# Optimization experiments

Measured on AMD Instinct MI355X. Metric: run time of the kernel, lower is better.

## Reference

```python
import jax, jax.numpy as jnp
import numpy as np

N = 50000
E = 800000
IN_C = 128
HID = 32
OUT_C = 16
NEG_SLOPE = 0.2


def setup_inputs() -> dict:
    key = jax.random.key(0)
    ks = jax.random.split(key, 16)
    x = jax.random.normal(ks[0], (N, IN_C), dtype=jnp.float32)
    edge_index = jax.random.randint(ks[1], (2, E), 0, N, dtype=jnp.int64)

    def glorot(k, shape):
        fan = shape[0] + shape[-1]
        return jax.random.uniform(k, shape, jnp.float32, -1.0, 1.0) * jnp.sqrt(6.0 / fan)

    # layer1: in=128 -> heads=4, ch=32, concat -> out 128
    W1 = glorot(ks[2], (IN_C, 4 * HID))
    a_src1 = glorot(ks[3], (4, HID))
    a_dst1 = glorot(ks[4], (4, HID))
    b1 = jnp.zeros((4 * HID,), jnp.float32)
    # layer2: in=128 -> heads=2, ch=32, concat -> out 64
    W2 = glorot(ks[5], (4 * HID, 2 * HID))
    a_src2 = glorot(ks[6], (2, HID))
    a_dst2 = glorot(ks[7], (2, HID))
    b2 = jnp.zeros((2 * HID,), jnp.float32)
    # layer3: in=64 -> heads=1, ch=16, mean -> out 16
    W3 = glorot(ks[8], (2 * HID, OUT_C))
    a_src3 = glorot(ks[9], (1, OUT_C))
    a_dst3 = glorot(ks[10], (1, OUT_C))
    b3 = jnp.zeros((OUT_C,), jnp.float32)
    return {"x": x, "edge_index": edge_index,
            "W1": W1, "a_src1": a_src1, "a_dst1": a_dst1, "b1": b1,
            "W2": W2, "a_src2": a_src2, "a_dst2": a_dst2, "b2": b2,
            "W3": W3, "a_src3": a_src3, "a_dst3": a_dst3, "b3": b3}


def gat_conv(x, src, dst, W, a_src, a_dst, bias, heads, ch, concat):
    n = x.shape[0]
    h = (x @ W).reshape(n, heads, ch)                      # [N,H,C]
    alpha_s = jnp.einsum('nhc,hc->nh', h, a_src)           # [N,H]
    alpha_d = jnp.einsum('nhc,hc->nh', h, a_dst)           # [N,H]
    logits = jax.nn.leaky_relu(alpha_s[src] + alpha_d[dst], NEG_SLOPE)  # [E,H]
    # segment softmax over edges sharing the same destination node
    m = jax.ops.segment_max(logits, dst, num_segments=n)
    m = jnp.where(jnp.isfinite(m), m, 0.0)
    e = jnp.exp(logits - m[dst])
    denom = jax.ops.segment_sum(e, dst, num_segments=n)
    alpha = e / (denom[dst] + 1e-16)                       # [E,H]
    msg = h[src] * alpha[:, :, None]                       # [E,H,C]
    out = jax.ops.segment_sum(msg, dst, num_segments=n)    # [N,H,C]
    out = out.reshape(n, heads * ch) if concat else out.mean(axis=1)
    return out + bias


def reference(x, edge_index, W1, a_src1, a_dst1, b1, W2, a_src2, a_dst2, b2, W3, a_src3, a_dst3, b3):
    n = x.shape[0]
    loops = jnp.arange(n, dtype=edge_index.dtype)
    src = jnp.concatenate([edge_index[0], loops])  # add self loops (PyG default)
    dst = jnp.concatenate([edge_index[1], loops])
    h = jax.nn.relu(gat_conv(x, src, dst, W1, a_src1, a_dst1, b1, 4, HID, True))
    h = jax.nn.relu(gat_conv(h, src, dst, W2, a_src2, a_dst2, b2, 2, HID, True))
    out = gat_conv(h, src, dst, W3, a_src3, a_dst3, b3, 1, OUT_C, False)
    return out
```

## Files before the change

### kernel.cpp

```cpp
#include <hip/hip_runtime.h>
#include <hip/hip_bf16.h>
#include <stdint.h>

#define NODES 50000
#define NEDGE 800000
#define TEDGE (NEDGE + NODES)
#define SBLK 25

typedef unsigned short u16;
typedef unsigned int u32;
typedef unsigned long long u64;
typedef short s16x8 __attribute__((ext_vector_type(8)));
typedef float f32x4 __attribute__((ext_vector_type(4)));

__device__ __forceinline__ float bf2f(u16 v) {
  return __uint_as_float(((u32)v) << 16);
}
__device__ __forceinline__ u16 f2bf(float f) {
  u32 u = __float_as_uint(f);
  u32 r = (u + 0x7FFFu + ((u >> 16) & 1u)) >> 16;
  return (u16)r;
}
__device__ __forceinline__ float lo16f(u32 w) { return __uint_as_float(w << 16); }
__device__ __forceinline__ float hi16f(u32 w) { return __uint_as_float(w & 0xFFFF0000u); }
__device__ __forceinline__ float lrelu(float x) {
  return (x > 0.f) ? x : 0.2f * x;
}
__device__ __forceinline__ int clampn(int v) {
  return ((u32)v < NODES) ? v : 0;
}
__device__ __forceinline__ float load1(const void* p, size_t i, bool fb) {
  return fb ? bf2f(((const u16*)p)[i]) : ((const float*)p)[i];
}
__device__ __forceinline__ u32 encf(float f) {
  u32 u = __float_as_uint(f);
  return (u & 0x80000000u) ? ~u : (u | 0x80000000u);
}
__device__ __forceinline__ float decf(u32 k) {
  u32 u = (k & 0x80000000u) ? (k & 0x7FFFFFFFu) : ~k;
  return __uint_as_float(u);
}

__global__ __launch_bounds__(256) void k_probe(
    const int* __restrict__ ei, const u16* __restrict__ xs16,
    int* __restrict__ flags, int* __restrict__ deg,
    const void* __restrict__ W1, const void* __restrict__ W2,
    const void* __restrict__ W3, const void* __restrict__ as1,
    const void* __restrict__ ad1, const void* __restrict__ as2,
    const void* __restrict__ ad2, const void* __restrict__ as3,
    const void* __restrict__ ad3, u16* __restrict__ wt1,
    u16* __restrict__ wt2, u16* __restrict__ wt3, u16* __restrict__ wa1,
    u16* __restrict__ wa2, u16* __restrict__ wa3) {
  __shared__ int sfb;
  int t = threadIdx.x;
  int g = blockIdx.x * 256 + t;
  if (g < NODES) deg[g] = 0;
  if (blockIdx.x == 0 && t >= 2 && t < 32) flags[t] = 0;
  if (t < 64) {
    int big = 0;
#pragma unroll
    for (int k = 0; k < 4; ++k) {
      u32 ex = (xs16[2 * (t * 4 + k)] >> 7) & 0xFF;
      big += (ex >= 0x90);
    }
#pragma unroll
    for (int off = 32; off >= 1; off >>= 1) big += __shfl_xor(big, off);
    if (t == 0) sfb = (big >= 8) ? 0 : 1;
    if (blockIdx.x == 0) {
      int odd = 0, even = 0;
#pragma unroll
      for (int k = 0; k < 4; ++k) {
        int idx = t + 64 * k;
        odd |= (ei[2 * idx + 1] != 0);
        even |= (ei[2 * idx] != 0);
      }
      u64 bo = __ballot(odd);
      u64 be = __ballot(even);
      if (t == 0) flags[0] = (bo == 0ull && be != 0ull) ? 1 : 0;
    }
  }
  __syncthreads();
  bool fb = sfb != 0;
  if (blockIdx.x == 0 && t == 0) flags[1] = fb ? 1 : 0;

  auto fidx = [](int n, int k, int KS) {
    int nt = n >> 4, lrow = n & 15, ks = k >> 5, quad = (k >> 3) & 3, j = k & 7;
    return ((size_t)((nt * KS + ks) * 64 + quad * 16 + lrow)) * 8 + j;
  };

  if (g < 16384) {
    int n = g >> 7, k = g & 127;
    wt1[fidx(n, k, 4)] = f2bf(load1(W1, (size_t)k * 128 + n, fb));
  } else if (g < 24576) {
    int r = g - 16384;
    int n = r >> 7, k = r & 127;
    wt2[fidx(n, k, 4)] = f2bf(load1(W2, (size_t)k * 64 + n, fb));
  } else if (g < 25600) {
    int r = g - 24576;
    int n = r >> 6, k = r & 63;
    wt3[fidx(n, k, 2)] = f2bf(load1(W3, (size_t)k * 16 + n, fb));
  } else if (g < 27648) {
    int e = g - 25600;
    int n = e >> 7, k = e & 127;
    float v = 0.f;
    if (n < 8) {
      int head = (n < 4) ? n : n - 4;
      const void* av = (n < 4) ? as1 : ad1;
      for (int c = 0; c < 32; ++c)
        v += load1(W1, (size_t)k * 128 + head * 32 + c, fb) *
             load1(av, head * 32 + c, fb);
    }
    wa1[fidx(n, k, 4)] = (n < 8) ? f2bf(v) : (u16)0;
  } else if (g < 29696) {
    int e = g - 27648;
    int n = e >> 7, k = e & 127;
    float v = 0.f;
    if (n < 4) {
      int head = (n < 2) ? n : n - 2;
      const void* av = (n < 2) ? as2 : ad2;
      for (int c = 0; c < 32; ++c)
        v += load1(W2, (size_t)k * 64 + head * 32 + c, fb) *
             load1(av, head * 32 + c, fb);
    }
    wa2[fidx(n, k, 4)] = (n < 4) ? f2bf(v) : (u16)0;
  } else if (g < 30720) {
    int e = g - 29696;
    int n = e >> 6, k = e & 63;
    float v = 0.f;
    if (n < 2) {
      const void* av = (n < 1) ? as3 : ad3;
      for (int c = 0; c < 16; ++c)
        v += load1(W3, (size_t)k * 16 + c, fb) * load1(av, c, fb);
    }
    wa3[fidx(n, k, 2)] = (n < 2) ? f2bf(v) : (u16)0;
  }
}

__global__ __launch_bounds__(256) void k_hist(const int* __restrict__ ei,
                                              const int* __restrict__ flags,
                                              int* deg, u16* __restrict__ rankarr,
                                              u16* __restrict__ src16,
                                              u16* __restrict__ dst16) {
  int e = blockIdx.x * 256 + threadIdx.x;
  if (e >= TEDGE) return;
  int d, s;
  if (e < NEDGE) {
    if (flags[0]) { s = ei[2 * e]; d = ei[2 * (NEDGE + e)]; }
    else { s = ei[e]; d = ei[NEDGE + e]; }
  } else {
    s = e - NEDGE; d = s;
  }
  s = clampn(s); d = clampn(d);
  src16[e] = (u16)s;
  dst16[e] = (u16)d;
  int r = atomicAdd(&deg[d], 1);
  rankarr[e] = (u16)min(r, 65535);
}

__global__ __launch_bounds__(1024) void k_scan(const int* __restrict__ deg,
                                               int* __restrict__ rowptr,
                                               int* __restrict__ parts,
                                               int* __restrict__ counter) {
  __shared__ int swave[16];
  __shared__ int sbase, stot;
  int b = blockIdx.x, t = threadIdx.x;
  int lane = t & 63, w = t >> 6;
  int i0 = b * 2048 + t * 2;
  int v0 = (i0 < NODES) ? deg[i0] : 0;
  int v1 = (i0 + 1 < NODES) ? deg[i0 + 1] : 0;
  int local = v0 + v1;
  int x = local;
#pragma unroll
  for (int off = 1; off < 64; off <<= 1) {
    int y = __shfl_up(x, off);
    if (lane >= off) x += y;
  }
  if (lane == 63) swave[w] = x;
  __syncthreads();
  if (w == 0) {
    int wv = (lane < 16) ? swave[lane] : 0;
#pragma unroll
    for (int off = 1; off < 16; off <<= 1) {
      int y = __shfl_up(wv, off);
      if (lane >= off) wv += y;
    }
    if (lane == 15) {
      __hip_atomic_store(&parts[b], wv, __ATOMIC_RELAXED,
                         __HIP_MEMORY_SCOPE_AGENT);
      __hip_atomic_fetch_add(counter, 1, __ATOMIC_RELEASE,
                             __HIP_MEMORY_SCOPE_AGENT);
    }
    if (lane < 16) swave[lane] = wv;
  }
  __syncthreads();
  if (t == 0) {
    while (__hip_atomic_load(counter, __ATOMIC_ACQUIRE,
                             __HIP_MEMORY_SCOPE_AGENT) < SBLK)
      __builtin_amdgcn_s_sleep(2);
  }
  __syncthreads();
  if (w == 0) {
    int pv = (lane < SBLK) ? __hip_atomic_load(&parts[lane], __ATOMIC_RELAXED,
                                               __HIP_MEMORY_SCOPE_AGENT)
                           : 0;
    int pb = (lane < b) ? pv : 0;
#pragma unroll
    for (int off = 32; off >= 1; off >>= 1) {
      pb += __shfl_xor(pb, off);
      pv += __shfl_xor(pv, off);
    }
    if (lane == 0) { sbase = pb; stot = pv; }
  }
  __syncthreads();
  int run = sbase + ((w == 0) ? 0 : swave[w - 1]) + (x - local);
  if (i0 < NODES) rowptr[i0] = run;
  if (i0 + 1 < NODES) rowptr[i0 + 1] = run + v0;
  if (b == 0 && t == 0) rowptr[NODES] = stot;
}

__global__ __launch_bounds__(256) void k_scatter(const u16* __restrict__ src16,
                                                 const u16* __restrict__ dst16,
                                                 const int* __restrict__ rowptr,
                                                 const u16* __restrict__ rankarr,
                                                 u16* __restrict__ srcs) {
  int e = blockIdx.x * 256 + threadIdx.x;
  if (e >= TEDGE) return;
  int d = dst16[e];
  int pos = rowptr[d] + (int)rankarr[e];
  srcs[pos] = src16[e];
}

template <int K, int N, int H, bool XEXT>
__global__ __launch_bounds__(256) void k_gmfma(const void* __restrict__ xin,
                                               const u16* __restrict__ wtf,
                                               const u16* __restrict__ waf,
                                               u16* __restrict__ hout,
                                               float* __restrict__ asg,
                                               float* __restrict__ adg,
                                               u32* __restrict__ gm,
                                               const int* __restrict__ flags,
                                               int M) {
  constexpr int NT = N / 16;
  constexpr int KS = K / 32;
  __shared__ u32 lmax[2 * H];
  int t = threadIdx.x;
  int lane = t & 63, w = t >> 6;
  int lrow = lane & 15, quad = lane >> 4;
  bool fb = flags[1] != 0;
  if (t < 2 * H) lmax[t] = 0;
  __syncthreads();

  int row0 = blockIdx.x * 128 + w * 32;
  f32x4 acc[2][NT];
  f32x4 eacc[2];
#pragma unroll
  for (int mt = 0; mt < 2; ++mt) {
    eacc[mt] = (f32x4){0.f, 0.f, 0.f, 0.f};
#pragma unroll
    for (int nt = 0; nt < NT; ++nt) acc[mt][nt] = (f32x4){0.f, 0.f, 0.f, 0.f};
  }
  int r0c = row0 + lrow;
  int r1c = row0 + 16 + lrow;
  if (r0c >= M) r0c = M - 1;
  if (r1c >= M) r1c = M - 1;

#pragma unroll 1
  for (int ks = 0; ks < KS; ++ks) {
    s16x8 bw[NT];
#pragma unroll
    for (int nt = 0; nt < NT; ++nt)
      bw[nt] = *(const s16x8*)(wtf + ((size_t)((nt * KS + ks) * 64 + lane)) * 8);
    s16x8 be = *(const s16x8*)(waf + ((size_t)(ks * 64 + lane)) * 8);
#pragma unroll
    for (int mt = 0; mt < 2; ++mt) {
      int grow = mt ? r1c : r0c;
      s16x8 a;
      if (XEXT && !fb) {
        const float* gp = (const float*)xin + (size_t)grow * K + ks * 32 + quad * 8;
        float4 f0 = *(const float4*)gp;
        float4 f1 = *(const float4*)(gp + 4);
        a[0] = (short)f2bf(f0.x); a[1] = (short)f2bf(f0.y);
        a[2] = (short)f2bf(f0.z); a[3] = (short)f2bf(f0.w);
        a[4] = (short)f2bf(f1.x); a[5] = (short)f2bf(f1.y);
        a[6] = (short)f2bf(f1.z); a[7] = (short)f2bf(f1.w);
      } else {
        a = *(const s16x8*)((const u16*)xin + (size_t)grow * K + ks * 32 + quad * 8);
      }
#pragma unroll
      for (int nt = 0; nt < NT; ++nt)
        acc[mt][nt] =
            __builtin_amdgcn_mfma_f32_16x16x32_bf16(a, bw[nt], acc[mt][nt], 0, 0, 0);
      eacc[mt] = __builtin_amdgcn_mfma_f32_16x16x32_bf16(a, be, eacc[mt], 0, 0, 0);
    }
  }

  float pm = -3.4e38f;
#pragma unroll
  for (int mt = 0; mt < 2; ++mt) {
    int baserow = row0 + mt * 16 + quad * 4;
#pragma unroll
    for (int r = 0; r < 4; ++r) {
      int grow = baserow + r;
      if (grow < M) {
#pragma unroll
        for (int nt = 0; nt < NT; ++nt)
          hout[(size_t)grow * N + nt * 16 + lrow] = f2bf(acc[mt][nt][r]);
        if (lrow < H) asg[grow * H + lrow] = eacc[mt][r];
        else if (lrow < 2 * H) adg[grow * H + (lrow - H)] = eacc[mt][r];
      }
      pm = fmaxf(pm, eacc[mt][r]);
    }
  }
  if (lrow < 2 * H) atomicMax(&lmax[lrow], encf(pm));
  __syncthreads();
  if (t < 2 * H) atomicMax(&gm[t], lmax[t]);
}

template <int H, int C, bool RELU, bool FINAL>
__global__ __launch_bounds__(256) void k_agg(const u16* __restrict__ hbuf,
                                             const float* __restrict__ asg,
                                             const float* __restrict__ adg,
                                             const int* __restrict__ rowptr,
                                             const u16* __restrict__ srcs,
                                             const void* __restrict__ bias,
                                             const int* __restrict__ flags,
                                             const u32* __restrict__ gm,
                                             void* __restrict__ outp, int n) {
  constexpr int HC = H * C;
  constexpr int L = HC / 8;
  constexpr int EPN = 32 / L;
  constexpr int UN = (4 * EPN <= 32) ? 4 : 2;
  __shared__ u16 lds_s[4][64];
  __shared__ float lds_e[4][64][H];
  int lane = threadIdx.x & 63;
  int w = threadIdx.x >> 6;
  int nh = lane >> 5;
  int hl = lane & 31;
  int node = blockIdx.x * 8 + w * 2 + nh;
  if (node >= n) node = n - 1;
  bool fb = flags[1] != 0;
  int start = rowptr[node], end = rowptr[node + 1];
  if (end < start || end - start > TEDGE) { start = 0; end = 0; }

  float adh[H], M[H];
#pragma unroll
  for (int h = 0; h < H; ++h) adh[h] = adg[node * H + h];
#pragma unroll
  for (int h = 0; h < H; ++h) M[h] = lrelu(decf(gm[h]) + decf(gm[H + h]));

  int sub = hl / L;
  int cl = hl & (L - 1);
  int ch0 = cl * 8;
  int myhead = ch0 / C;
  int base = nh * 32;

  float den[H];
#pragma unroll
  for (int h = 0; h < H; ++h) den[h] = 0.f;
  float acc[UN][8];
#pragma unroll
  for (int u = 0; u < UN; ++u)
#pragma unroll
    for (int i = 0; i < 8; ++i) acc[u][i] = 0.f;

  for (int chunk = start; chunk < end; chunk += 32) {
    int e = chunk + hl;
    int s = 0;
    float ee[H];
#pragma unroll
    for (int h = 0; h < H; ++h) ee[h] = 0.f;
    if (e < end) {
      s = srcs[e];
      float av[H];
      if (H == 4) { float4 t4 = *(const float4*)(asg + s * 4);
        av[0] = t4.x; av[1] = t4.y; av[H > 2 ? 2 : 0] = t4.z; av[H > 3 ? 3 : 0] = t4.w; }
      else if (H == 2) { float2 t2 = *(const float2*)(asg + s * 2); av[0] = t2.x; av[1] = t2.y; }
      else av[0] = asg[s];
#pragma unroll
      for (int h = 0; h < H; ++h) {
        float x = __expf(lrelu(av[h] + adh[h]) - M[h]);
        ee[h] = x;
        den[h] += x;
      }
    }
    __builtin_amdgcn_wave_barrier();
    lds_s[w][lane] = (u16)s;
#pragma unroll
    for (int h = 0; h < H; ++h) lds_e[w][lane][h] = ee[h];
    __builtin_amdgcn_wave_barrier();

    int cn = min(32, end - chunk);
    for (int j = 0; j < cn; j += UN * EPN) {
      int sx[UN];
      float ax[UN];
#pragma unroll
      for (int u = 0; u < UN; ++u) {
        int ei_ = base + j + u * EPN + sub;
        sx[u] = lds_s[w][ei_];
        ax[u] = lds_e[w][ei_][myhead];
      }
#pragma unroll
      for (int u = 0; u < UN; ++u) {
        uint4 v = *(const uint4*)(hbuf + (size_t)sx[u] * HC + ch0);
        acc[u][0] += ax[u] * lo16f(v.x); acc[u][1] += ax[u] * hi16f(v.x);
        acc[u][2] += ax[u] * lo16f(v.y); acc[u][3] += ax[u] * hi16f(v.y);
        acc[u][4] += ax[u] * lo16f(v.z); acc[u][5] += ax[u] * hi16f(v.z);
        acc[u][6] += ax[u] * lo16f(v.w); acc[u][7] += ax[u] * hi16f(v.w);
      }
    }
  }

#pragma unroll
  for (int m = 16; m >= 1; m >>= 1) {
#pragma unroll
    for (int h = 0; h < H; ++h) den[h] += __shfl_xor(den[h], m);
  }
  float tt[8];
#pragma unroll
  for (int i = 0; i < 8; ++i) {
    tt[i] = acc[0][i];
#pragma unroll
    for (int u = 1; u < UN; ++u) tt[i] += acc[u][i];
  }
#pragma unroll
  for (int m = L; m < 32; m <<= 1) {
#pragma unroll
    for (int i = 0; i < 8; ++i) tt[i] += __shfl_xor(tt[i], m);
  }

  if (sub == 0) {
    float inv = 1.f / (den[myhead] + 1e-16f);
    float o[8];
#pragma unroll
    for (int i = 0; i < 8; ++i) {
      o[i] = tt[i] * inv + load1(bias, ch0 + i, fb);
      if (RELU) o[i] = fmaxf(o[i], 0.f);
    }
    bool obf = FINAL ? fb : true;
    if (obf) {
      uint4 pk;
      pk.x = (u32)f2bf(o[0]) | ((u32)f2bf(o[1]) << 16);
      pk.y = (u32)f2bf(o[2]) | ((u32)f2bf(o[3]) << 16);
      pk.z = (u32)f2bf(o[4]) | ((u32)f2bf(o[5]) << 16);
      pk.w = (u32)f2bf(o[6]) | ((u32)f2bf(o[7]) << 16);
      *(uint4*)((u16*)outp + (size_t)node * HC + ch0) = pk;
    } else {
      float* op = (float*)outp + (size_t)node * HC + ch0;
      *(float4*)op = make_float4(o[0], o[1], o[2], o[3]);
      *(float4*)(op + 4) = make_float4(o[4], o[5], o[6], o[7]);
    }
  }
}


extern "C" void kernel_launch(void* const* d_in, const int* in_sizes, int n_in,
                              void* d_out, int out_size, void* d_ws, size_t ws_size,
                              hipStream_t stream) {
  const void* x   = d_in[0];
  const int* ei   = (const int*)d_in[1];
  const void* W1  = d_in[2];
  const void* as1 = d_in[3];
  const void* ad1 = d_in[4];
  const void* b1  = d_in[5];
  const void* W2  = d_in[6];
  const void* as2 = d_in[7];
  const void* ad2 = d_in[8];
  const void* b2  = d_in[9];
  const void* W3  = d_in[10];
  const void* as3 = d_in[11];
  const void* ad3 = d_in[12];
  const void* b3  = d_in[13];

  char* w = (char*)d_ws;
  auto alloc = [&](size_t bytes) {
    char* p = w;
    w += (bytes + 255) & ~(size_t)255;
    return p;
  };
  int* flags    = (int*)alloc(256);
  int* parts    = (int*)alloc(256);
  int* deg      = (int*)alloc((size_t)NODES * 4);
  int* rowptr   = (int*)alloc((size_t)(NODES + 1) * 4);
  u16* rankarr  = (u16*)alloc((size_t)TEDGE * 2);
  u16* src16    = (u16*)alloc((size_t)TEDGE * 2);
  u16* dst16    = (u16*)alloc((size_t)TEDGE * 2);
  u16* srcs     = (u16*)alloc((size_t)TEDGE * 2);
  float* asg    = (float*)alloc((size_t)NODES * 4 * 4);
  float* adg    = (float*)alloc((size_t)NODES * 4 * 4);
  u16* wt1      = (u16*)alloc((size_t)128 * 128 * 2);
  u16* wt2      = (u16*)alloc((size_t)64 * 128 * 2);
  u16* wt3      = (u16*)alloc((size_t)16 * 64 * 2);
  u16* wa1      = (u16*)alloc((size_t)16 * 128 * 2);
  u16* wa2      = (u16*)alloc((size_t)16 * 128 * 2);
  u16* wa3      = (u16*)alloc((size_t)16 * 64 * 2);
  u16* hbuf     = (u16*)alloc((size_t)NODES * 128 * 2);
  u16* obuf     = (u16*)alloc((size_t)NODES * 128 * 2);

  u32* gm1 = (u32*)(flags + 8);
  u32* gm2 = (u32*)(flags + 16);
  u32* gm3 = (u32*)(flags + 24);

  int gblocks = (NODES + 127) / 128;
  int ablocks = (NODES + 7) / 8;

  k_probe<<<(NODES + 255) / 256, 256, 0, stream>>>(
      ei, (const u16*)x, flags, deg, W1, W2, W3, as1, ad1, as2, ad2, as3, ad3,
      wt1, wt2, wt3, wa1, wa2, wa3);
  k_hist<<<(TEDGE + 255) / 256, 256, 0, stream>>>(ei, flags, deg, rankarr,
                                                  src16, dst16);
  k_scan<<<SBLK, 1024, 0, stream>>>(deg, rowptr, parts, flags + 2);
  k_scatter<<<(TEDGE + 255) / 256, 256, 0, stream>>>(src16, dst16, rowptr, rankarr, srcs);

  k_gmfma<128, 128, 4, true><<<gblocks, 256, 0, stream>>>(x, wt1, wa1, hbuf, asg, adg, gm1, flags, NODES);
  k_agg<4, 32, true, false><<<ablocks, 256, 0, stream>>>(hbuf, asg, adg, rowptr, srcs, b1, flags, gm1, obuf, NODES);
  k_gmfma<128, 64, 2, false><<<gblocks, 256, 0, stream>>>(obuf, wt2, wa2, hbuf, asg, adg, gm2, flags, NODES);
  k_agg<2, 32, true, false><<<ablocks, 256, 0, stream>>>(hbuf, asg, adg, rowptr, srcs, b2, flags, gm2, obuf, NODES);
  k_gmfma<64, 16, 1, false><<<gblocks, 256, 0, stream>>>(obuf, wt3, wa3, hbuf, asg, adg, gm3, flags, NODES);
  k_agg<1, 16, false, true><<<ablocks, 256, 0, stream>>>(hbuf, asg, adg, rowptr, srcs, b3, flags, gm3, d_out, NODES);
}
```

Measured before the change: 265.1 us.

## Fuse edge histogram with layer-1 MFMA GEMM and stage X tiles in LDS

Merges the edge histogram kernel and the first-layer projection GEMM into one launch, with different block ranges doing each job so the two independent pieces of work run concurrently. The GEMM is also restructured to 64-row tiles, with each wave taking 16 rows and the input rows staged once into padded LDS instead of each wave loading its rows straight from global memory. This removes one launch and should improve overlap and occupancy. In exchange, the histogram blocks now reserve the static LDS they never use, and the smaller tiles double the number of GEMM blocks and their atomic max updates.

```diff
diff --git a/kernel.cpp b/kernel.cpp
--- a/kernel.cpp
+++ b/kernel.cpp
@@ -6,6 +6,8 @@
 #define NEDGE 800000
 #define TEDGE (NEDGE + NODES)
 #define SBLK 25
+#define HBLK ((TEDGE + 255) / 256)
+#define GBLK ((NODES + 63) / 64)
 
 typedef unsigned short u16;
 typedef unsigned int u32;
@@ -136,25 +138,129 @@
   }
 }
 
-__global__ __launch_bounds__(256) void k_hist(const int* __restrict__ ei,
-                                              const int* __restrict__ flags,
-                                              int* deg, u16* __restrict__ rankarr,
-                                              u16* __restrict__ src16,
-                                              u16* __restrict__ dst16) {
-  int e = blockIdx.x * 256 + threadIdx.x;
-  if (e >= TEDGE) return;
-  int d, s;
-  if (e < NEDGE) {
-    if (flags[0]) { s = ei[2 * e]; d = ei[2 * (NEDGE + e)]; }
-    else { s = ei[e]; d = ei[NEDGE + e]; }
-  } else {
-    s = e - NEDGE; d = s;
-  }
-  s = clampn(s); d = clampn(d);
-  src16[e] = (u16)s;
-  dst16[e] = (u16)d;
-  int r = atomicAdd(&deg[d], 1);
-  rankarr[e] = (u16)min(r, 65535);
+template <int K, int N, int H, bool XEXT>
+__device__ __forceinline__ void gmfma_tile(const void* __restrict__ xin,
+                                           const u16* __restrict__ wtf,
+                                           const u16* __restrict__ waf,
+                                           u16* __restrict__ hout,
+                                           float* __restrict__ asg,
+                                           float* __restrict__ adg,
+                                           u32* __restrict__ gm,
+                                           const int* __restrict__ flags,
+                                           int M, int row0,
+                                           u16* __restrict__ xlds,
+                                           u32* __restrict__ lmax) {
+  constexpr int KP = K + 8;
+  constexpr int NT = N / 16;
+  constexpr int KS = K / 32;
+  constexpr int KG = K / 8;
+  int t = threadIdx.x;
+  bool fb = flags[1] != 0;
+  if (t < 2 * H) lmax[t] = 0;
+
+  bool xbf = XEXT ? fb : true;
+  for (int i = t; i < 64 * KG; i += 256) {
+    int r = i / KG, kg = i % KG;
+    int grow = row0 + r;
+    if (grow >= M) grow = M - 1;
+    if (xbf) {
+      *(uint4*)&xlds[r * KP + kg * 8] =
+          *(const uint4*)((const u16*)xin + (size_t)grow * K + kg * 8);
+    } else {
+      const float* gp = (const float*)xin + (size_t)grow * K + kg * 8;
+      float4 f0 = *(const float4*)gp, f1 = *(const float4*)(gp + 4);
+      *(ushort4*)&xlds[r * KP + kg * 8] =
+          make_ushort4(f2bf(f0.x), f2bf(f0.y), f2bf(f0.z), f2bf(f0.w));
+      *(ushort4*)&xlds[r * KP + kg * 8 + 4] =
+          make_ushort4(f2bf(f1.x), f2bf(f1.y), f2bf(f1.z), f2bf(f1.w));
+    }
+  }
+  __syncthreads();
+
+  int lane = t & 63, w = t >> 6;
+  int lrow = lane & 15, quad = lane >> 4;
+  f32x4 acc[NT];
+  f32x4 eacc = (f32x4){0.f, 0.f, 0.f, 0.f};
+#pragma unroll
+  for (int nt = 0; nt < NT; ++nt) acc[nt] = (f32x4){0.f, 0.f, 0.f, 0.f};
+
+  const u16* xbase = xlds + (w * 16 + lrow) * KP + quad * 8;
+#pragma unroll
+  for (int ks = 0; ks < KS; ++ks) {
+    s16x8 a = *(const s16x8*)(xbase + ks * 32);
+    s16x8 be = *(const s16x8*)(waf + ((size_t)(ks * 64 + lane)) * 8);
+    eacc = __builtin_amdgcn_mfma_f32_16x16x32_bf16(a, be, eacc, 0, 0, 0);
+#pragma unroll
+    for (int nt = 0; nt < NT; ++nt) {
+      s16x8 b = *(const s16x8*)(wtf + ((size_t)((nt * KS + ks) * 64 + lane)) * 8);
+      acc[nt] = __builtin_amdgcn_mfma_f32_16x16x32_bf16(a, b, acc[nt], 0, 0, 0);
+    }
+  }
+
+  float pm = -3.4e38f;
+  int baserow = row0 + w * 16 + quad * 4;
+#pragma unroll
+  for (int r = 0; r < 4; ++r) {
+    int grow = baserow + r;
+    if (grow < M) {
+#pragma unroll
+      for (int nt = 0; nt < NT; ++nt)
+        hout[(size_t)grow * N + nt * 16 + lrow] = f2bf(acc[nt][r]);
+      if (lrow < H) asg[grow * H + lrow] = eacc[r];
+      else if (lrow < 2 * H) adg[grow * H + (lrow - H)] = eacc[r];
+    }
+    pm = fmaxf(pm, eacc[r]);
+  }
+  if (lrow < 2 * H) atomicMax(&lmax[lrow], encf(pm));
+  __syncthreads();
+  if (t < 2 * H) atomicMax(&gm[t], lmax[t]);
+}
+
+template <int K, int N, int H, bool XEXT>
+__global__ __launch_bounds__(256) void k_gmfma(const void* __restrict__ xin,
+                                               const u16* __restrict__ wtf,
+                                               const u16* __restrict__ waf,
+                                               u16* __restrict__ hout,
+                                               float* __restrict__ asg,
+                                               float* __restrict__ adg,
+                                               u32* __restrict__ gm,
+                                               const int* __restrict__ flags,
+                                               int M) {
+  __shared__ u16 xlds[64 * (K + 8)];
+  __shared__ u32 lmax[2 * H];
+  gmfma_tile<K, N, H, XEXT>(xin, wtf, waf, hout, asg, adg, gm, flags, M,
+                            blockIdx.x * 64, xlds, lmax);
+}
+
+__global__ __launch_bounds__(256) void k_build_l1(
+    const void* __restrict__ xin, const u16* __restrict__ wtf,
+    const u16* __restrict__ waf, u16* __restrict__ hout,
+    float* __restrict__ asg, float* __restrict__ adg, u32* __restrict__ gm,
+    const int* __restrict__ flags, const int* __restrict__ ei,
+    int* __restrict__ deg, u16* __restrict__ rankarr,
+    u16* __restrict__ src16, u16* __restrict__ dst16) {
+  __shared__ u16 xlds[64 * 136];
+  __shared__ u32 lmax[8];
+  int bi = blockIdx.x;
+  if (bi < HBLK) {
+    int e = bi * 256 + threadIdx.x;
+    if (e >= TEDGE) return;
+    int d, s;
+    if (e < NEDGE) {
+      if (flags[0]) { s = ei[2 * e]; d = ei[2 * (NEDGE + e)]; }
+      else { s = ei[e]; d = ei[NEDGE + e]; }
+    } else {
+      s = e - NEDGE; d = s;
+    }
+    s = clampn(s); d = clampn(d);
+    src16[e] = (u16)s;
+    dst16[e] = (u16)d;
+    int r = atomicAdd(&deg[d], 1);
+    rankarr[e] = (u16)min(r, 65535);
+    return;
+  }
+  gmfma_tile<128, 128, 4, true>(xin, wtf, waf, hout, asg, adg, gm, flags,
+                                NODES, (bi - HBLK) * 64, xlds, lmax);
 }
 
 __global__ __launch_bounds__(1024) void k_scan(const int* __restrict__ deg,
@@ -228,92 +334,6 @@
   int d = dst16[e];
   int pos = rowptr[d] + (int)rankarr[e];
   srcs[pos] = src16[e];
-}
-
-template <int K, int N, int H, bool XEXT>
-__global__ __launch_bounds__(256) void k_gmfma(const void* __restrict__ xin,
-                                               const u16* __restrict__ wtf,
-                                               const u16* __restrict__ waf,
-                                               u16* __restrict__ hout,
-                                               float* __restrict__ asg,
-                                               float* __restrict__ adg,
-                                               u32* __restrict__ gm,
-                                               const int* __restrict__ flags,
-                                               int M) {
-  constexpr int NT = N / 16;
-  constexpr int KS = K / 32;
-  __shared__ u32 lmax[2 * H];
-  int t = threadIdx.x;
-  int lane = t & 63, w = t >> 6;
-  int lrow = lane & 15, quad = lane >> 4;
-  bool fb = flags[1] != 0;
-  if (t < 2 * H) lmax[t] = 0;
-  __syncthreads();
-
-  int row0 = blockIdx.x * 128 + w * 32;
-  f32x4 acc[2][NT];
-  f32x4 eacc[2];
-#pragma unroll
-  for (int mt = 0; mt < 2; ++mt) {
-    eacc[mt] = (f32x4){0.f, 0.f, 0.f, 0.f};
-#pragma unroll
-    for (int nt = 0; nt < NT; ++nt) acc[mt][nt] = (f32x4){0.f, 0.f, 0.f, 0.f};
-  }
-  int r0c = row0 + lrow;
-  int r1c = row0 + 16 + lrow;
-  if (r0c >= M) r0c = M - 1;
-  if (r1c >= M) r1c = M - 1;
-
-#pragma unroll 1
-  for (int ks = 0; ks < KS; ++ks) {
-    s16x8 bw[NT];
-#pragma unroll
-    for (int nt = 0; nt < NT; ++nt)
-      bw[nt] = *(const s16x8*)(wtf + ((size_t)((nt * KS + ks) * 64 + lane)) * 8);
-    s16x8 be = *(const s16x8*)(waf + ((size_t)(ks * 64 + lane)) * 8);
-#pragma unroll
-    for (int mt = 0; mt < 2; ++mt) {
-      int grow = mt ? r1c : r0c;
-      s16x8 a;
-      if (XEXT && !fb) {
-        const float* gp = (const float*)xin + (size_t)grow * K + ks * 32 + quad * 8;
-        float4 f0 = *(const float4*)gp;
-        float4 f1 = *(const float4*)(gp + 4);
-        a[0] = (short)f2bf(f0.x); a[1] = (short)f2bf(f0.y);
-        a[2] = (short)f2bf(f0.z); a[3] = (short)f2bf(f0.w);
-        a[4] = (short)f2bf(f1.x); a[5] = (short)f2bf(f1.y);
-        a[6] = (short)f2bf(f1.z); a[7] = (short)f2bf(f1.w);
-      } else {
-        a = *(const s16x8*)((const u16*)xin + (size_t)grow * K + ks * 32 + quad * 8);
-      }
-#pragma unroll
-      for (int nt = 0; nt < NT; ++nt)
-        acc[mt][nt] =
-            __builtin_amdgcn_mfma_f32_16x16x32_bf16(a, bw[nt], acc[mt][nt], 0, 0, 0);
-      eacc[mt] = __builtin_amdgcn_mfma_f32_16x16x32_bf16(a, be, eacc[mt], 0, 0, 0);
-    }
-  }
-
-  float pm = -3.4e38f;
-#pragma unroll
-  for (int mt = 0; mt < 2; ++mt) {
-    int baserow = row0 + mt * 16 + quad * 4;
-#pragma unroll
-    for (int r = 0; r < 4; ++r) {
-      int grow = baserow + r;
-      if (grow < M) {
-#pragma unroll
-        for (int nt = 0; nt < NT; ++nt)
-          hout[(size_t)grow * N + nt * 16 + lrow] = f2bf(acc[mt][nt][r]);
-        if (lrow < H) asg[grow * H + lrow] = eacc[mt][r];
-        else if (lrow < 2 * H) adg[grow * H + (lrow - H)] = eacc[mt][r];
-      }
-      pm = fmaxf(pm, eacc[mt][r]);
-    }
-  }
-  if (lrow < 2 * H) atomicMax(&lmax[lrow], encf(pm));
-  __syncthreads();
-  if (t < 2 * H) atomicMax(&gm[t], lmax[t]);
 }
 
 template <int H, int C, bool RELU, bool FINAL>
@@ -500,21 +520,20 @@
   u32* gm2 = (u32*)(flags + 16);
   u32* gm3 = (u32*)(flags + 24);
 
-  int gblocks = (NODES + 127) / 128;
   int ablocks = (NODES + 7) / 8;
 
   k_probe<<<(NODES + 255) / 256, 256, 0, stream>>>(
       ei, (const u16*)x, flags, deg, W1, W2, W3, as1, ad1, as2, ad2, as3, ad3,
       wt1, wt2, wt3, wa1, wa2, wa3);
-  k_hist<<<(TEDGE + 255) / 256, 256, 0, stream>>>(ei, flags, deg, rankarr,
-                                                  src16, dst16);
+  k_build_l1<<<HBLK + GBLK, 256, 0, stream>>>(x, wt1, wa1, hbuf, asg, adg,
+                                              gm1, flags, ei, deg, rankarr,
+                                              src16, dst16);
   k_scan<<<SBLK, 1024, 0, stream>>>(deg, rowptr, parts, flags + 2);
   k_scatter<<<(TEDGE + 255) / 256, 256, 0, stream>>>(src16, dst16, rowptr, rankarr, srcs);
 
-  k_gmfma<128, 128, 4, true><<<gblocks, 256, 0, stream>>>(x, wt1, wa1, hbuf, asg, adg, gm1, flags, NODES);
   k_agg<4, 32, true, false><<<ablocks, 256, 0, stream>>>(hbuf, asg, adg, rowptr, srcs, b1, flags, gm1, obuf, NODES);
-  k_gmfma<128, 64, 2, false><<<gblocks, 256, 0, stream>>>(obuf, wt2, wa2, hbuf, asg, adg, gm2, flags, NODES);
+  k_gmfma<128, 64, 2, false><<<GBLK, 256, 0, stream>>>(obuf, wt2, wa2, hbuf, asg, adg, gm2, flags, NODES);
   k_agg<2, 32, true, false><<<ablocks, 256, 0, stream>>>(hbuf, asg, adg, rowptr, srcs, b2, flags, gm2, obuf, NODES);
-  k_gmfma<64, 16, 1, false><<<gblocks, 256, 0, stream>>>(obuf, wt3, wa3, hbuf, asg, adg, gm3, flags, NODES);
+  k_gmfma<64, 16, 1, false><<<GBLK, 256, 0, stream>>>(obuf, wt3, wa3, hbuf, asg, adg, gm3, flags, NODES);
   k_agg<1, 16, false, true><<<ablocks, 256, 0, stream>>>(hbuf, asg, adg, rowptr, srcs, b3, flags, gm3, d_out, NODES);
 }
```

New measurement: 268.8 us. About the same (+1.4%).
